# Optimization experiments

Measured on AMD Instinct MI355X. Metric: run time of the kernel, lower is better.

The kernel has to match this reference:

```python
import jax, jax.numpy as jnp
import numpy as np

B, L, D = 2, 2048, 512
NUM_HEADS = 8
LN_EPS = 1e-5


def setup_inputs() -> dict:
    key = jax.random.key(0)
    ks = jax.random.split(key, 4)
    s = 1.0 / np.sqrt(D)
    return {
        "x": jax.random.normal(ks[0], (B, L, D), dtype=jnp.float32),
        "in_proj_w": jax.random.normal(ks[1], (3 * D, D), dtype=jnp.float32) * s,
        "in_proj_b": jnp.zeros((3 * D,), dtype=jnp.float32),
        "out_proj_w": jax.random.normal(ks[2], (D, D), dtype=jnp.float32) * s,
        "out_proj_b": jnp.zeros((D,), dtype=jnp.float32),
        "ln_gamma": jnp.ones((D,), dtype=jnp.float32),
        "ln_beta": jnp.zeros((D,), dtype=jnp.float32),
        "window_size": 10,
    }


def reference(x, in_proj_w, in_proj_b, out_proj_w, out_proj_b, ln_gamma, ln_beta, window_size):
    b, l, d = x.shape
    h = NUM_HEADS
    hd = d // h

    # packed qkv projection (torch Linear: y = x @ W.T + b)
    qkv = x @ in_proj_w.T + in_proj_b  # [B, L, 3D]
    q, k, v = jnp.split(qkv, 3, axis=-1)

    def heads(t):  # [B, L, D] -> [B, H, L, hd]
        return t.reshape(b, l, h, hd).transpose(0, 2, 1, 3)

    q, k, v = heads(q), heads(k), heads(v)
    q = q * (1.0 / np.sqrt(hd))  # torch MHA scales q

    scores = jnp.einsum("bhqd,bhkd->bhqk", q, k)  # [B, H, L, L]

    # Faithful to the source + torch bool attn_mask semantics:
    # mask starts all-True, positions OUTSIDE window set to False;
    # torch masks (=-inf) where the bool mask is True, i.e. INSIDE
    # the window [i - w//2, i + w//2).
    half = window_size // 2
    i = jnp.arange(l)[:, None]
    j = jnp.arange(l)[None, :]
    banned = (j >= i - half) & (j < i + half)  # [L, L] bool
    scores = jnp.where(banned[None, None], -jnp.inf, scores)

    attn = jax.nn.softmax(scores, axis=-1)
    ctx = jnp.einsum("bhqk,bhkd->bhqd", attn, v)  # [B, H, L, hd]
    ctx = ctx.transpose(0, 2, 1, 3).reshape(b, l, d)
    attn_out = ctx @ out_proj_w.T + out_proj_b

    # residual + LayerNorm
    y = x + attn_out
    mu = jnp.mean(y, axis=-1, keepdims=True)
    var = jnp.mean(jnp.square(y - mu), axis=-1, keepdims=True)
    return (y - mu) * jax.lax.rsqrt(var + LN_EPS) * ln_gamma + ln_beta
```

## Files before the change

kernel.cpp:

```cpp
#include <hip/hip_runtime.h>
#include <hip/hip_bf16.h>
#include <math.h>

namespace {

constexpr int Bb = 2, Ll = 2048, Dd = 512, Hh = 8;
constexpr int M = Bb * Ll;
constexpr int THREE_D = 3 * Dd;

typedef __attribute__((ext_vector_type(8))) short short8;
typedef __attribute__((ext_vector_type(4))) short short4v;
typedef __attribute__((ext_vector_type(4))) float f32x4;

__device__ __forceinline__ unsigned short f2bf(float x) {
  union { __hip_bfloat16 h; unsigned short u; } cv;
  cv.h = __float2bfloat16(x);
  return cv.u;
}

__device__ __forceinline__ void gload_lds16(const void* g, void* l) {
  __builtin_amdgcn_global_load_lds(
      (const __attribute__((address_space(1))) void*)g,
      (__attribute__((address_space(3))) void*)l, 16, 0, 0);
}

constexpr int QUADS_X = (M * Dd) / 4;
constexpr int QUADS_W1 = (THREE_D * Dd) / 4;
constexpr int QUADS_W2 = (Dd * Dd) / 4;
constexpr int QUADS_TOT = QUADS_X + QUADS_W1 + QUADS_W2;

__global__ __launch_bounds__(256) void cvt_bf16(
    const float* __restrict__ x, const float* __restrict__ w1,
    const float* __restrict__ w2, unsigned short* __restrict__ xb,
    unsigned short* __restrict__ wb, unsigned short* __restrict__ wob) {
  const int i = blockIdx.x * 256 + threadIdx.x;
  const float* src;
  unsigned short* dst;
  if (i < QUADS_X) {
    src = x + 4 * (size_t)i;
    dst = xb + 4 * (size_t)i;
  } else if (i < QUADS_X + QUADS_W1) {
    const int j = i - QUADS_X;
    src = w1 + 4 * (size_t)j;
    dst = wb + 4 * (size_t)j;
  } else {
    const int j = i - (QUADS_X + QUADS_W1);
    src = w2 + 4 * (size_t)j;
    dst = wob + 4 * (size_t)j;
  }
  float4 v = *reinterpret_cast<const float4*>(src);
  ushort4 o;
  o.x = f2bf(v.x); o.y = f2bf(v.y); o.z = f2bf(v.z); o.w = f2bf(v.w);
  *reinterpret_cast<ushort4*>(dst) = o;
}

template <int K, int N, bool QKV>
__global__ __launch_bounds__(256) void gemm_mfma(
    const unsigned short* __restrict__ A, const unsigned short* __restrict__ B,
    const float* __restrict__ bias, const float* __restrict__ R,
    unsigned short* __restrict__ Cb, float* __restrict__ Cf) {
  __shared__ unsigned short As[128 * 64];
  __shared__ unsigned short Bs[128 * 64];

  const int tid = threadIdx.x;
  const int lane = tid & 63;
  const int wu = __builtin_amdgcn_readfirstlane(tid >> 6);
  const int q = lane & 15;
  const int g = lane >> 4;
  const int wr = wu >> 1, wc = wu & 1;
  const int m0 = blockIdx.y * 128, n0 = blockIdx.x * 128;

  const int srow = lane >> 3;
  const int scol = 8 * ((lane & 7) ^ srow);
  const unsigned short* Ag = A + (size_t)(m0 + 32 * wu + srow) * K + scol;
  const unsigned short* Bg = B + (size_t)(n0 + 32 * wu + srow) * K + scol;
  char* AsW = (char*)As + wu * 4096;
  char* BsW = (char*)Bs + wu * 4096;

  f32x4 acc[4][4] = {};

  for (int k0 = 0; k0 < K; k0 += 64) {
    __syncthreads();
#pragma unroll
    for (int i = 0; i < 4; ++i) {
      gload_lds16(Ag + (size_t)(8 * i) * K + k0, AsW + 1024 * i);
      gload_lds16(Bg + (size_t)(8 * i) * K + k0, BsW + 1024 * i);
    }
    __syncthreads();

    const char* Abase = (const char*)As + (wr * 64 + q) * 128;
    const char* Bbase = (const char*)Bs + (wc * 64 + q) * 128;
#pragma unroll
    for (int s = 0; s < 2; ++s) {
      const int csw = (64 * s + 16 * g) ^ ((q & 7) << 4);
      short8 af[4], bf[4];
#pragma unroll
      for (int m = 0; m < 4; ++m)
        af[m] = *reinterpret_cast<const short8*>(Abase + m * 2048 + csw);
#pragma unroll
      for (int n = 0; n < 4; ++n)
        bf[n] = *reinterpret_cast<const short8*>(Bbase + n * 2048 + csw);
#pragma unroll
      for (int m = 0; m < 4; ++m)
#pragma unroll
        for (int n = 0; n < 4; ++n)
          acc[m][n] = __builtin_amdgcn_mfma_f32_16x16x32_bf16(
              af[m], bf[n], acc[m][n], 0, 0, 0);
    }
  }

  const float sc = (QKV && n0 < Dd) ? 0.125f : 1.0f;
#pragma unroll
  for (int m = 0; m < 4; ++m) {
#pragma unroll
    for (int r = 0; r < 4; ++r) {
      const int row = m0 + wr * 64 + m * 16 + 4 * g + r;
#pragma unroll
      for (int n = 0; n < 4; ++n) {
        const int col = n0 + wc * 64 + n * 16 + q;
        const float v = acc[m][n][r] + bias[col];
        if (QKV) {
          Cb[(size_t)row * N + col] = f2bf(v * sc);
        } else {
          Cf[(size_t)row * N + col] = v + R[(size_t)row * N + col];
        }
      }
    }
  }
}

__global__ __launch_bounds__(512) void attn_mfma(
    const unsigned short* __restrict__ qkv, const int* __restrict__ wsz,
    unsigned short* __restrict__ ctx) {
  __shared__ unsigned short Kls[8192];
  __shared__ unsigned short Vls[8192];
  __shared__ unsigned short Pls[8192];

  const int tid = threadIdx.x;
  const int lane = tid & 63;
  const int w = tid >> 6;
  const int wu = __builtin_amdgcn_readfirstlane(w);
  const int wg = wu & 3;
  const int hv = wu >> 2;
  const int q = lane & 15;
  const int g = lane >> 4;

  const int qt = blockIdx.x & 31;
  const int h = (blockIdx.x >> 5) & 7;
  const int b = blockIdx.x >> 8;
  const int qbase = qt * 64;
  const int hwin = wsz[0] >> 1;

  const size_t bh_base = (size_t)b * Ll * THREE_D + h * 64;

  const unsigned short* qrow =
      qkv + bh_base + (size_t)(qbase + wg * 16 + q) * THREE_D;
  short8 qf0 = *reinterpret_cast<const short8*>(qrow + 8 * g);
  short8 qf1 = *reinterpret_cast<const short8*>(qrow + 32 + 8 * g);
  asm volatile("s_waitcnt vmcnt(0)" : "+v"(qf0), "+v"(qf1)::"memory");

  const int k_rowoff = wg * 16 + (lane >> 3);
  const int k_dcol = 8 * ((lane & 7) ^ ((lane >> 3) & 7));
  const unsigned short* kg_base = qkv + bh_base + Dd + k_dcol;

  const int v_rowoff = 32 * (wg >> 1) + 8 * ((lane >> 4) & 3) +
                       4 * ((lane >> 3) & 1) + ((lane >> 1) & 3);
  const unsigned short* vg_base = qkv + bh_base + 2 * Dd + 8 * (lane & 1);

  unsigned short* kst = &Kls[hv * 4096 + wg * 1024];
  unsigned short* vst = &Vls[hv * 4096 + wg * 1024];
  unsigned short* pw = &Pls[wu * 1024];
  const char* kbytes = (const char*)Kls + hv * 8192;
  const char* vbytes = (const char*)Vls + hv * 8192;
  char* pb = (char*)pw;

  f32x4 oacc[4] = {};
  float m_run = -1e30f, l_run = 0.f;

  const int qlo = qbase + wg * 16;
  const int iq = qlo + q;

  for (int t = 0; t < 16; ++t) {
    const int kbase = (hv * 16 + t) * 64;
    __syncthreads();

    gload_lds16(kg_base + (size_t)(kbase + k_rowoff) * THREE_D, kst);
    gload_lds16(kg_base + (size_t)(kbase + k_rowoff + 8) * THREE_D, kst + 512);
    gload_lds16(vg_base + (size_t)(kbase + v_rowoff) * THREE_D +
                    16 * ((2 * wg + 0) & 3), vst);
    gload_lds16(vg_base + (size_t)(kbase + v_rowoff) * THREE_D +
                    16 * ((2 * wg + 1) & 3), vst + 512);
    __syncthreads();

    f32x4 sa[4] = {};
    __builtin_amdgcn_s_setprio(1);
#pragma unroll
    for (int s = 0; s < 2; ++s) {
      const short8 qf = s ? qf1 : qf0;
#pragma unroll
      for (int n = 0; n < 4; ++n) {
        const int baddr =
            (((16 * n + q) * 128 + 64 * s + 16 * g)) ^ ((q & 7) << 4);
        const short8 kf = *reinterpret_cast<const short8*>(kbytes + baddr);
        sa[n] = __builtin_amdgcn_mfma_f32_16x16x32_bf16(kf, qf, sa[n], 0, 0, 0);
      }
    }
    __builtin_amdgcn_s_setprio(0);

    if (kbase + 64 > qlo - hwin && kbase < qlo + 15 + hwin) {
#pragma unroll
      for (int n = 0; n < 4; ++n) {
#pragma unroll
        for (int r = 0; r < 4; ++r) {
          const int j = kbase + 16 * n + 4 * g + r;
          if (j >= iq - hwin && j < iq + hwin) sa[n][r] = -1e30f;
        }
      }
    }

    const float mx0 = fmaxf(fmaxf(sa[0][0], sa[0][1]), fmaxf(sa[0][2], sa[0][3]));
    const float mx1 = fmaxf(fmaxf(sa[1][0], sa[1][1]), fmaxf(sa[1][2], sa[1][3]));
    const float mx2 = fmaxf(fmaxf(sa[2][0], sa[2][1]), fmaxf(sa[2][2], sa[2][3]));
    const float mx3 = fmaxf(fmaxf(sa[3][0], sa[3][1]), fmaxf(sa[3][2], sa[3][3]));
    float mx = fmaxf(fmaxf(mx0, mx1), fmaxf(mx2, mx3));
    mx = fmaxf(mx, __shfl_xor(mx, 16));
    mx = fmaxf(mx, __shfl_xor(mx, 32));
    const float mnew = fmaxf(m_run, mx);
    const float corr = __expf(m_run - mnew);
    m_run = mnew;
#pragma unroll
    for (int n = 0; n < 4; ++n)
#pragma unroll
      for (int r = 0; r < 4; ++r) sa[n][r] = __expf(sa[n][r] - mnew);
    const float s0 = (sa[0][0] + sa[0][1]) + (sa[0][2] + sa[0][3]);
    const float s1 = (sa[1][0] + sa[1][1]) + (sa[1][2] + sa[1][3]);
    const float s2 = (sa[2][0] + sa[2][1]) + (sa[2][2] + sa[2][3]);
    const float s3 = (sa[3][0] + sa[3][1]) + (sa[3][2] + sa[3][3]);
    float ps = (s0 + s1) + (s2 + s3);
    ps += __shfl_xor(ps, 16);
    ps += __shfl_xor(ps, 32);
    l_run = l_run * corr + ps;

    float corr_o[4];
#pragma unroll
    for (int r = 0; r < 4; ++r) corr_o[r] = __shfl(corr, 4 * g + r, 16);
#pragma unroll
    for (int n = 0; n < 4; ++n)
#pragma unroll
      for (int r = 0; r < 4; ++r) oacc[n][r] *= corr_o[r];

#pragma unroll
    for (int n = 0; n < 4; ++n) {
      uint2 pk;
      pk.x = (unsigned)f2bf(sa[n][0]) | ((unsigned)f2bf(sa[n][1]) << 16);
      pk.y = (unsigned)f2bf(sa[n][2]) | ((unsigned)f2bf(sa[n][3]) << 16);
      *reinterpret_cast<uint2*>(
          pb + q * 128 + ((32 * n + 8 * g) ^ ((q & 7) << 4))) = pk;
    }
    asm volatile("s_waitcnt lgkmcnt(0)" ::: "memory");

#pragma unroll
    for (int s = 0; s < 2; ++s) {
      const short8 pf = *reinterpret_cast<const short8*>(
          pb + q * 128 + ((64 * s + 16 * g) ^ ((q & 7) << 4)));
      short4v vlo[4], vhi[4];
#pragma unroll
      for (int n = 0; n < 4; ++n) {
        const __attribute__((address_space(3))) unsigned short* va =
            (const __attribute__((address_space(3))) unsigned short*)(
                vbytes + 4096 * s + 1024 * n + 256 * g + 8 * q);
        asm volatile("ds_read_b64_tr_b16 %0, %1 offset:0" : "=v"(vlo[n]) : "v"(va));
        asm volatile("ds_read_b64_tr_b16 %0, %1 offset:128" : "=v"(vhi[n]) : "v"(va));
      }
      asm volatile("s_waitcnt lgkmcnt(0)"
                   : "+v"(vlo[0]), "+v"(vhi[0]), "+v"(vlo[1]), "+v"(vhi[1]),
                     "+v"(vlo[2]), "+v"(vhi[2]), "+v"(vlo[3]), "+v"(vhi[3])
                   :
                   : "memory");
      __builtin_amdgcn_sched_barrier(0);
      __builtin_amdgcn_s_setprio(1);
#pragma unroll
      for (int n = 0; n < 4; ++n) {
        const short8 vf =
            __builtin_shufflevector(vlo[n], vhi[n], 0, 1, 2, 3, 4, 5, 6, 7);
        oacc[n] = __builtin_amdgcn_mfma_f32_16x16x32_bf16(pf, vf, oacc[n], 0, 0, 0);
      }
      __builtin_amdgcn_s_setprio(0);
    }
  }

  float* Om = (float*)Kls;
  float* mls = (float*)Vls;

  __syncthreads();
  if (w >= 4) {
#pragma unroll
    for (int r = 0; r < 4; ++r) {
      const int rr = wg * 16 + 4 * g + r;
#pragma unroll
      for (int n = 0; n < 4; ++n) Om[rr * 64 + 16 * n + q] = oacc[n][r];
    }
    if (g == 0)
      *reinterpret_cast<float2*>(&mls[(wg * 16 + q) * 2]) =
          make_float2(m_run, l_run);
  }
  __syncthreads();
  if (w < 4) {
#pragma unroll
    for (int r = 0; r < 4; ++r) {
      const int rr = wg * 16 + 4 * g + r;
      const float m_own = __shfl(m_run, 4 * g + r, 16);
      const float l_own = __shfl(l_run, 4 * g + r, 16);
      const float2 ml2 = *reinterpret_cast<const float2*>(&mls[rr * 2]);
      const float ms = fmaxf(m_own, ml2.x);
      const float c1 = __expf(m_own - ms);
      const float c2 = __expf(ml2.x - ms);
      const float inv = 1.0f / (c1 * l_own + c2 * ml2.y);
      const int row = qbase + rr;
      unsigned short* crow = ctx + ((size_t)(b * Ll + row)) * Dd + h * 64 + q;
#pragma unroll
      for (int n = 0; n < 4; ++n) {
        const float o2 = Om[rr * 64 + 16 * n + q];
        crow[16 * n] = f2bf((c1 * oacc[n][r] + c2 * o2) * inv);
      }
    }
  }
}

__global__ __launch_bounds__(256) void ln_kernel(
    const float* __restrict__ y, const float* __restrict__ gamma,
    const float* __restrict__ beta, float* __restrict__ out) {
  const int row = blockIdx.x;
  const int tid = threadIdx.x;
  const float* yr = y + (size_t)row * Dd;

  float2 v = *reinterpret_cast<const float2*>(&yr[tid * 2]);
  float s = v.x + v.y;
  float qq = v.x * v.x + v.y * v.y;
#pragma unroll
  for (int off = 1; off < 64; off <<= 1) {
    s += __shfl_xor(s, off, 64);
    qq += __shfl_xor(qq, off, 64);
  }
  __shared__ float ss[4], qs[4];
  if ((tid & 63) == 0) { ss[tid >> 6] = s; qs[tid >> 6] = qq; }
  __syncthreads();
  s = (ss[0] + ss[1]) + (ss[2] + ss[3]);
  qq = (qs[0] + qs[1]) + (qs[2] + qs[3]);

  const float mu = s * (1.0f / Dd);
  const float var = qq * (1.0f / Dd) - mu * mu;
  const float rstd = rsqrtf(var + 1e-5f);

  float2 gmv = *reinterpret_cast<const float2*>(&gamma[tid * 2]);
  float2 bev = *reinterpret_cast<const float2*>(&beta[tid * 2]);
  float2 o;
  o.x = (v.x - mu) * rstd * gmv.x + bev.x;
  o.y = (v.y - mu) * rstd * gmv.y + bev.y;
  *reinterpret_cast<float2*>(&out[(size_t)row * Dd + tid * 2]) = o;
}

}

extern "C" void kernel_launch(void* const* d_in, const int* in_sizes, int n_in,
                              void* d_out, int out_size, void* d_ws,
                              size_t ws_size, hipStream_t stream) {
  const float* x = (const float*)d_in[0];
  const float* w_in = (const float*)d_in[1];
  const float* b_in = (const float*)d_in[2];
  const float* w_out = (const float*)d_in[3];
  const float* b_out = (const float*)d_in[4];
  const float* gamma = (const float*)d_in[5];
  const float* beta = (const float*)d_in[6];
  const int* wsz = (const int*)d_in[7];
  float* out = (float*)d_out;

  unsigned short* ws16 = (unsigned short*)d_ws;
  unsigned short* qkvb = ws16;
  unsigned short* ctxb = ws16 + 6291456;
  unsigned short* xb = ws16 + 8388608;
  unsigned short* wb = ws16 + 10485760;
  unsigned short* wob = ws16 + 11272192;
  float* y = (float*)d_ws;

  dim3 blk(256);

  cvt_bf16<<<dim3(QUADS_TOT / 256), blk, 0, stream>>>(x, w_in, w_out, xb, wb,
                                                      wob);
  gemm_mfma<512, 1536, true><<<dim3(12, 32), blk, 0, stream>>>(
      xb, wb, b_in, nullptr, qkvb, nullptr);
  attn_mfma<<<dim3(512), dim3(512), 0, stream>>>(qkvb, wsz, ctxb);
  gemm_mfma<512, 512, false><<<dim3(4, 32), blk, 0, stream>>>(
      ctxb, wob, b_out, x, nullptr, y);
  ln_kernel<<<dim3(M), blk, 0, stream>>>(y, gamma, beta, out);
}
```

Before: 80.37 us.

## Load K fragments directly to registers and prefetch next K/V tile

The attention kernel no longer stages K through shared memory. Each lane loads its MFMA K fragments straight from global memory into registers, and the next tile's K and V are prefetched into registers while the current tile is being computed. V is copied from registers into LDS after a barrier. This removes the K LDS buffer and the async global-to-LDS loads, and it sets a launch-bounds occupancy hint of 4 blocks. The trade-off is higher register pressure (eight short8 K fragments plus two V vectors per lane) and uncoalesced, duplicated K reads across the waves that share a head.

```diff
diff --git a/kernel.cpp b/kernel.cpp
--- a/kernel.cpp
+++ b/kernel.cpp
@@ -129,10 +129,9 @@
   }
 }
 
-__global__ __launch_bounds__(512) void attn_mfma(
+__global__ __launch_bounds__(512, 4) void attn_mfma(
     const unsigned short* __restrict__ qkv, const int* __restrict__ wsz,
     unsigned short* __restrict__ ctx) {
-  __shared__ unsigned short Kls[8192];
   __shared__ unsigned short Vls[8192];
   __shared__ unsigned short Pls[8192];
 
@@ -159,19 +158,21 @@
   short8 qf1 = *reinterpret_cast<const short8*>(qrow + 32 + 8 * g);
   asm volatile("s_waitcnt vmcnt(0)" : "+v"(qf0), "+v"(qf1)::"memory");
 
-  const int k_rowoff = wg * 16 + (lane >> 3);
-  const int k_dcol = 8 * ((lane & 7) ^ ((lane >> 3) & 7));
-  const unsigned short* kg_base = qkv + bh_base + Dd + k_dcol;
+  const unsigned short* kq =
+      qkv + bh_base + Dd + (size_t)q * THREE_D + 8 * g;
 
   const int v_rowoff = 32 * (wg >> 1) + 8 * ((lane >> 4) & 3) +
                        4 * ((lane >> 3) & 1) + ((lane >> 1) & 3);
-  const unsigned short* vg_base = qkv + bh_base + 2 * Dd + 8 * (lane & 1);
-
-  unsigned short* kst = &Kls[hv * 4096 + wg * 1024];
-  unsigned short* vst = &Vls[hv * 4096 + wg * 1024];
+  const unsigned short* vg0 =
+      qkv + bh_base + 2 * Dd + 8 * (lane & 1) + 16 * ((2 * wg + 0) & 3);
+  const unsigned short* vg1 =
+      qkv + bh_base + 2 * Dd + 8 * (lane & 1) + 16 * ((2 * wg + 1) & 3);
+
+  char* vw0 = (char*)Vls + hv * 8192 + wg * 2048 + 16 * lane;
+  char* vw1 = vw0 + 1024;
+  const char* vbytes = (const char*)Vls + hv * 8192;
+
   unsigned short* pw = &Pls[wu * 1024];
-  const char* kbytes = (const char*)Kls + hv * 8192;
-  const char* vbytes = (const char*)Vls + hv * 8192;
   char* pb = (char*)pw;
 
   f32x4 oacc[4] = {};
@@ -180,17 +181,28 @@
   const int qlo = qbase + wg * 16;
   const int iq = qlo + q;
 
+  short8 kfr[8];
+  short8 vr0, vr1;
+
+#define LOADK(kbase)                                                       \
+  {                                                                        \
+    _Pragma("unroll") for (int s = 0; s < 2; ++s)                          \
+        _Pragma("unroll") for (int n = 0; n < 4; ++n)                      \
+            kfr[s * 4 + n] = *reinterpret_cast<const short8*>(             \
+                kq + (size_t)((kbase) + 16 * n) * THREE_D + 32 * s);       \
+  }
+
+  const int kb0 = hv * 1024;
+  LOADK(kb0);
+  vr0 = *reinterpret_cast<const short8*>(vg0 + (size_t)(kb0 + v_rowoff) * THREE_D);
+  vr1 = *reinterpret_cast<const short8*>(vg1 + (size_t)(kb0 + v_rowoff) * THREE_D);
+  *reinterpret_cast<short8*>(vw0) = vr0;
+  *reinterpret_cast<short8*>(vw1) = vr1;
+  asm volatile("s_waitcnt lgkmcnt(0)" ::: "memory");
+  __builtin_amdgcn_s_barrier();
+
   for (int t = 0; t < 16; ++t) {
     const int kbase = (hv * 16 + t) * 64;
-    __syncthreads();
-
-    gload_lds16(kg_base + (size_t)(kbase + k_rowoff) * THREE_D, kst);
-    gload_lds16(kg_base + (size_t)(kbase + k_rowoff + 8) * THREE_D, kst + 512);
-    gload_lds16(vg_base + (size_t)(kbase + v_rowoff) * THREE_D +
-                    16 * ((2 * wg + 0) & 3), vst);
-    gload_lds16(vg_base + (size_t)(kbase + v_rowoff) * THREE_D +
-                    16 * ((2 * wg + 1) & 3), vst + 512);
-    __syncthreads();
 
     f32x4 sa[4] = {};
     __builtin_amdgcn_s_setprio(1);
@@ -198,14 +210,19 @@
     for (int s = 0; s < 2; ++s) {
       const short8 qf = s ? qf1 : qf0;
 #pragma unroll
-      for (int n = 0; n < 4; ++n) {
-        const int baddr =
-            (((16 * n + q) * 128 + 64 * s + 16 * g)) ^ ((q & 7) << 4);
-        const short8 kf = *reinterpret_cast<const short8*>(kbytes + baddr);
-        sa[n] = __builtin_amdgcn_mfma_f32_16x16x32_bf16(kf, qf, sa[n], 0, 0, 0);
-      }
+      for (int n = 0; n < 4; ++n)
+        sa[n] = __builtin_amdgcn_mfma_f32_16x16x32_bf16(kfr[s * 4 + n], qf,
+                                                        sa[n], 0, 0, 0);
     }
     __builtin_amdgcn_s_setprio(0);
+
+    if (t < 15) {
+      LOADK(kbase + 64);
+      vr0 = *reinterpret_cast<const short8*>(
+          vg0 + (size_t)(kbase + 64 + v_rowoff) * THREE_D);
+      vr1 = *reinterpret_cast<const short8*>(
+          vg1 + (size_t)(kbase + 64 + v_rowoff) * THREE_D);
+    }
 
     if (kbase + 64 > qlo - hwin && kbase < qlo + 15 + hwin) {
 #pragma unroll
@@ -287,9 +304,19 @@
       }
       __builtin_amdgcn_s_setprio(0);
     }
-  }
-
-  float* Om = (float*)Kls;
+
+    __builtin_amdgcn_s_barrier();
+
+    if (t < 15) {
+      *reinterpret_cast<short8*>(vw0) = vr0;
+      *reinterpret_cast<short8*>(vw1) = vr1;
+      asm volatile("s_waitcnt lgkmcnt(0)" ::: "memory");
+    }
+    __builtin_amdgcn_s_barrier();
+  }
+#undef LOADK
+
+  float* Om = (float*)Pls;
   float* mls = (float*)Vls;
 
   __syncthreads();
```

Result: slower. 113.8 us (+41.5%).

## Halve attention block size and add lazy softmax rescaling

Applied to the files above, without the earlier changes.

The attention kernel now uses 256-thread blocks that each cover 32 queries, launched as 1024 blocks. Each wave loads two K/V sub-tiles so the shared tiles stay the same size, and the P buffer shrinks. Online softmax now rescales the running max and the accumulators only when a new max exceeds the old one by more than 8, which skips the shuffle and rescale work on most tiles. Each block now loads the full K/V sequence for only 32 queries, doubling global K/V traffic. Skipping rescales relies on exp(s-m) staying bounded by e^8, which holds in fp32.

```diff
diff --git a/kernel.cpp b/kernel.cpp
--- a/kernel.cpp
+++ b/kernel.cpp
@@ -129,26 +129,26 @@
   }
 }
 
-__global__ __launch_bounds__(512) void attn_mfma(
+__global__ __launch_bounds__(256, 4) void attn_mfma(
     const unsigned short* __restrict__ qkv, const int* __restrict__ wsz,
     unsigned short* __restrict__ ctx) {
   __shared__ unsigned short Kls[8192];
   __shared__ unsigned short Vls[8192];
-  __shared__ unsigned short Pls[8192];
+  __shared__ unsigned short Pls[4096];
 
   const int tid = threadIdx.x;
   const int lane = tid & 63;
   const int w = tid >> 6;
   const int wu = __builtin_amdgcn_readfirstlane(w);
-  const int wg = wu & 3;
-  const int hv = wu >> 2;
+  const int wg = wu & 1;
+  const int hv = wu >> 1;
   const int q = lane & 15;
   const int g = lane >> 4;
 
-  const int qt = blockIdx.x & 31;
-  const int h = (blockIdx.x >> 5) & 7;
-  const int b = blockIdx.x >> 8;
-  const int qbase = qt * 64;
+  const int qt = blockIdx.x & 63;
+  const int h = (blockIdx.x >> 6) & 7;
+  const int b = blockIdx.x >> 9;
+  const int qbase = qt * 32;
   const int hwin = wsz[0] >> 1;
 
   const size_t bh_base = (size_t)b * Ll * THREE_D + h * 64;
@@ -159,19 +159,13 @@
   short8 qf1 = *reinterpret_cast<const short8*>(qrow + 32 + 8 * g);
   asm volatile("s_waitcnt vmcnt(0)" : "+v"(qf0), "+v"(qf1)::"memory");
 
-  const int k_rowoff = wg * 16 + (lane >> 3);
   const int k_dcol = 8 * ((lane & 7) ^ ((lane >> 3) & 7));
   const unsigned short* kg_base = qkv + bh_base + Dd + k_dcol;
-
-  const int v_rowoff = 32 * (wg >> 1) + 8 * ((lane >> 4) & 3) +
-                       4 * ((lane >> 3) & 1) + ((lane >> 1) & 3);
   const unsigned short* vg_base = qkv + bh_base + 2 * Dd + 8 * (lane & 1);
 
-  unsigned short* kst = &Kls[hv * 4096 + wg * 1024];
-  unsigned short* vst = &Vls[hv * 4096 + wg * 1024];
-  unsigned short* pw = &Pls[wu * 1024];
   const char* kbytes = (const char*)Kls + hv * 8192;
   const char* vbytes = (const char*)Vls + hv * 8192;
+  unsigned short* pw = &Pls[wu * 1024];
   char* pb = (char*)pw;
 
   f32x4 oacc[4] = {};
@@ -184,12 +178,21 @@
     const int kbase = (hv * 16 + t) * 64;
     __syncthreads();
 
-    gload_lds16(kg_base + (size_t)(kbase + k_rowoff) * THREE_D, kst);
-    gload_lds16(kg_base + (size_t)(kbase + k_rowoff + 8) * THREE_D, kst + 512);
-    gload_lds16(vg_base + (size_t)(kbase + v_rowoff) * THREE_D +
-                    16 * ((2 * wg + 0) & 3), vst);
-    gload_lds16(vg_base + (size_t)(kbase + v_rowoff) * THREE_D +
-                    16 * ((2 * wg + 1) & 3), vst + 512);
+#pragma unroll
+    for (int half = 0; half < 2; ++half) {
+      const int ow = wg + 2 * half;
+      const int krow = ow * 16 + (lane >> 3);
+      unsigned short* kd = &Kls[hv * 4096 + ow * 1024];
+      gload_lds16(kg_base + (size_t)(kbase + krow) * THREE_D, kd);
+      gload_lds16(kg_base + (size_t)(kbase + krow + 8) * THREE_D, kd + 512);
+      const int vro = 32 * (ow >> 1) + 8 * ((lane >> 4) & 3) +
+                      4 * ((lane >> 3) & 1) + ((lane >> 1) & 3);
+      unsigned short* vd = &Vls[hv * 4096 + ow * 1024];
+      gload_lds16(vg_base + (size_t)(kbase + vro) * THREE_D +
+                      16 * ((2 * ow + 0) & 3), vd);
+      gload_lds16(vg_base + (size_t)(kbase + vro) * THREE_D +
+                      16 * ((2 * ow + 1) & 3), vd + 512);
+    }
     __syncthreads();
 
     f32x4 sa[4] = {};
@@ -225,13 +228,23 @@
     float mx = fmaxf(fmaxf(mx0, mx1), fmaxf(mx2, mx3));
     mx = fmaxf(mx, __shfl_xor(mx, 16));
     mx = fmaxf(mx, __shfl_xor(mx, 32));
-    const float mnew = fmaxf(m_run, mx);
-    const float corr = __expf(m_run - mnew);
-    m_run = mnew;
+    if (!__all(mx <= m_run + 8.0f)) {
+      const float mnew = fmaxf(m_run, mx);
+      const float corr = __expf(m_run - mnew);
+      m_run = mnew;
+      l_run *= corr;
+      float corr_o[4];
+#pragma unroll
+      for (int r = 0; r < 4; ++r) corr_o[r] = __shfl(corr, 4 * g + r, 16);
+#pragma unroll
+      for (int n = 0; n < 4; ++n)
+#pragma unroll
+        for (int r = 0; r < 4; ++r) oacc[n][r] *= corr_o[r];
+    }
 #pragma unroll
     for (int n = 0; n < 4; ++n)
 #pragma unroll
-      for (int r = 0; r < 4; ++r) sa[n][r] = __expf(sa[n][r] - mnew);
+      for (int r = 0; r < 4; ++r) sa[n][r] = __expf(sa[n][r] - m_run);
     const float s0 = (sa[0][0] + sa[0][1]) + (sa[0][2] + sa[0][3]);
     const float s1 = (sa[1][0] + sa[1][1]) + (sa[1][2] + sa[1][3]);
     const float s2 = (sa[2][0] + sa[2][1]) + (sa[2][2] + sa[2][3]);
@@ -239,15 +252,7 @@
     float ps = (s0 + s1) + (s2 + s3);
     ps += __shfl_xor(ps, 16);
     ps += __shfl_xor(ps, 32);
-    l_run = l_run * corr + ps;
-
-    float corr_o[4];
-#pragma unroll
-    for (int r = 0; r < 4; ++r) corr_o[r] = __shfl(corr, 4 * g + r, 16);
-#pragma unroll
-    for (int n = 0; n < 4; ++n)
-#pragma unroll
-      for (int r = 0; r < 4; ++r) oacc[n][r] *= corr_o[r];
+    l_run += ps;
 
 #pragma unroll
     for (int n = 0; n < 4; ++n) {
@@ -289,11 +294,11 @@
     }
   }
 
-  float* Om = (float*)Kls;
+  float* Om = (float*)Pls;
   float* mls = (float*)Vls;
 
   __syncthreads();
-  if (w >= 4) {
+  if (w >= 2) {
 #pragma unroll
     for (int r = 0; r < 4; ++r) {
       const int rr = wg * 16 + 4 * g + r;
@@ -305,7 +310,7 @@
           make_float2(m_run, l_run);
   }
   __syncthreads();
-  if (w < 4) {
+  if (w < 2) {
 #pragma unroll
     for (int r = 0; r < 4; ++r) {
       const int rr = wg * 16 + 4 * g + r;
@@ -389,7 +394,7 @@
                                                       wob);
   gemm_mfma<512, 1536, true><<<dim3(12, 32), blk, 0, stream>>>(
       xb, wb, b_in, nullptr, qkvb, nullptr);
-  attn_mfma<<<dim3(512), dim3(512), 0, stream>>>(qkvb, wsz, ctxb);
+  attn_mfma<<<dim3(1024), blk, 0, stream>>>(qkvb, wsz, ctxb);
   gemm_mfma<512, 512, false><<<dim3(4, 32), blk, 0, stream>>>(
       ctxb, wob, b_out, x, nullptr, y);
   ln_kernel<<<dim3(M), blk, 0, stream>>>(y, gamma, beta, out);
```

After: 83.00 us. +3.3%, slower.
